# Optimization experiments

Measured on AMD Instinct MI355X. Metric: run time of the kernel, lower is better.

Reference implementation:

```python
import jax, jax.numpy as jnp
import numpy as np

HALF = 24576          # per-side HalfKP features (64 king sq * 6 piece * 64 sq)
NUMEL = 2 * HALF      # util.half_kp_numel()
BASE = 128
B = 8192


def _linear(x, W, b):
    return x @ W.T + b


def setup_inputs() -> dict:
    key = jax.random.key(0)
    ks = jax.random.split(key, 16)
    s = 0.01
    return {
        "pov": jax.random.uniform(ks[0], (B, 1), dtype=jnp.float32),
        "white": jax.random.uniform(ks[1], (B, HALF), dtype=jnp.float32),
        "black": jax.random.uniform(ks[2], (B, HALF), dtype=jnp.float32),
        "w_aff_W": jax.random.normal(ks[3], (BASE, NUMEL), dtype=jnp.float32) * s,
        "w_aff_b": jax.random.normal(ks[4], (BASE,), dtype=jnp.float32) * s,
        "b_aff_W": jax.random.normal(ks[5], (BASE, NUMEL), dtype=jnp.float32) * s,
        "b_aff_b": jax.random.normal(ks[6], (BASE,), dtype=jnp.float32) * s,
        "fc0_W": jax.random.normal(ks[7], (32, 2 * BASE), dtype=jnp.float32) * s,
        "fc0_b": jax.random.normal(ks[8], (32,), dtype=jnp.float32) * s,
        "fc1_W": jax.random.normal(ks[9], (32, 32), dtype=jnp.float32) * s,
        "fc1_b": jax.random.normal(ks[10], (32,), dtype=jnp.float32) * s,
        "fc2_W": jax.random.normal(ks[11], (32, 64), dtype=jnp.float32) * s,
        "fc2_b": jax.random.normal(ks[12], (32,), dtype=jnp.float32) * s,
        "fc3_W": jax.random.normal(ks[13], (1, 96), dtype=jnp.float32) * s,
        "fc3_b": jax.random.normal(ks[14], (1,), dtype=jnp.float32) * s,
    }


def reference(pov, white, black, w_aff_W, w_aff_b, b_aff_W, b_aff_b,
              fc0_W, fc0_b, fc1_W, fc1_b, fc2_W, fc2_b, fc3_W, fc3_b):
    # util.half_kp(a, b) = cat([a, b], dim=1)
    w_feat = jnp.concatenate([white, black], axis=1)  # [B, NUMEL]
    b_feat = jnp.concatenate([black, white], axis=1)
    w_ = _linear(w_feat, w_aff_W, w_aff_b)            # [B, 128]
    b_ = _linear(b_feat, b_aff_W, b_aff_b)
    wb = jnp.concatenate([w_, b_], axis=1)            # [B, 256]
    bw = jnp.concatenate([b_, w_], axis=1)
    base = jax.nn.relu(pov * wb + (1.0 - pov) * bw)
    x = jax.nn.relu(_linear(base, fc0_W, fc0_b))      # [B, 32]
    x = jnp.concatenate([x, jax.nn.relu(_linear(x, fc1_W, fc1_b))], axis=1)  # [B, 64]
    x = jnp.concatenate([x, jax.nn.relu(_linear(x, fc2_W, fc2_b))], axis=1)  # [B, 96]
    return _linear(x, fc3_W, fc3_b)                   # [B, 1]
```

## Files before the change

kernel.cpp:

```cpp
#include <hip/hip_runtime.h>
#include <hip/hip_bf16.h>
#include <stdint.h>

typedef float f32x4 __attribute__((ext_vector_type(4)));
typedef float fvec4 __attribute__((ext_vector_type(4)));
typedef short bf16x8 __attribute__((ext_vector_type(8)));

#define HALF_K 24576
#define NUMELK 49152
#define BATCH  8192
#define BM 128
#define BN 256
#define BK 64

__device__ __forceinline__ short f2bf(float f) {
  __hip_bfloat16 h = __float2bfloat16(f);
  return __builtin_bit_cast(short, h);
}

__device__ __forceinline__ void gload_lds16(const short* g, short* l) {
  __builtin_amdgcn_global_load_lds(
      (const __attribute__((address_space(1))) unsigned*)g,
      (__attribute__((address_space(3))) unsigned*)l, 16, 0, 0);
}
__device__ __forceinline__ void gload_lds16f(const float* g, float* l) {
  __builtin_amdgcn_global_load_lds(
      (const __attribute__((address_space(1))) unsigned*)g,
      (__attribute__((address_space(3))) unsigned*)l, 16, 0, 0);
}

__global__ __launch_bounds__(256)
void nnue_prep(const float* __restrict__ wW, const float* __restrict__ bW,
               short* __restrict__ Bprep) {
  int gid = blockIdx.x * 256 + threadIdx.x;
  int KT  = gid >> 11;
  int rem = gid & 2047;
  int col = rem >> 3;
  int kc  = rem & 7;
  int kg  = KT * 64 + kc * 8;
  const float* src;
  if (col < 128) {
    src = wW + (size_t)col * NUMELK + kg;
  } else {
    int kk = (kg < HALF_K) ? (kg + HALF_K) : (kg - HALF_K);
    src = bW + (size_t)(col - 128) * NUMELK + kk;
  }
  fvec4 v0 = ((const fvec4*)src)[0];
  fvec4 v1 = ((const fvec4*)src)[1];
  bf16x8 o;
  o[0] = f2bf(v0[0]); o[1] = f2bf(v0[1]); o[2] = f2bf(v0[2]); o[3] = f2bf(v0[3]);
  o[4] = f2bf(v1[0]); o[5] = f2bf(v1[1]); o[6] = f2bf(v1[2]); o[7] = f2bf(v1[3]);
  *(bf16x8*)(Bprep + (size_t)KT * 16384 + col * 64 + ((kc ^ (col & 7)) << 3)) = o;
}

__global__ __launch_bounds__(512, 4)
void nnue_gemm(const float* __restrict__ white, const float* __restrict__ black,
               const short* __restrict__ Bprep, float* __restrict__ partial,
               int kchunk, int S) {
  __shared__ float Alds[BM * BK];
  __shared__ short Blds[BN * BK];

  const int t    = threadIdx.x;
  const int lane = t & 63;
  const int wid  = t >> 6;

  const int bid = blockIdx.x;
  const int xcd = bid & 7, bi = bid >> 3;
  const int xpk = 8 / S;
  const int ks  = xcd / xpk;
  const int mt  = (xcd % xpk) * (64 / xpk) + bi;
  const int m0  = mt * BM;
  const int k0  = ks * kchunk;

  f32x4 acc[4][4];
  const f32x4 zero = {0.f, 0.f, 0.f, 0.f};
#pragma unroll
  for (int a = 0; a < 4; ++a)
#pragma unroll
    for (int b = 0; b < 4; ++b) acc[a][b] = zero;

  const int wm = wid >> 2, wn = wid & 3;
  const int l15 = lane & 15, l4 = lane >> 4;
  const int achunk = lane & 15;
  const int arsub  = lane >> 4;

  auto issueDMA = [&](int kg) {
    const float* Af; int ka;
    if (kg < HALF_K) { Af = white; ka = kg; } else { Af = black; ka = kg - HALF_K; }
#pragma unroll
    for (int j = 0; j < 4; ++j) {
      int row = wid * 16 + j * 4 + arsub;
      int sc  = achunk ^ (row & 7);
      const float* src = Af + (size_t)(m0 + row) * HALF_K + ka + sc * 4;
      gload_lds16f(src, &Alds[(wid * 4 + j) * 256]);
    }
    const int KT = kg >> 6;
    const short* bsrc = Bprep + (size_t)KT * 16384 + wid * 2048 + lane * 8;
    short* bdst = &Blds[wid * 2048];
#pragma unroll
    for (int j = 0; j < 4; ++j)
      gload_lds16(bsrc + j * 512, bdst + j * 512);
  };

  auto compute = [&]() {
#pragma unroll
    for (int kstep = 0; kstep < 2; ++kstep) {
      const int kc = kstep * 4 + l4;
      bf16x8 bfr[4];
#pragma unroll
      for (int nf = 0; nf < 4; ++nf) {
        int col = wn * 64 + nf * 16 + l15;
        bfr[nf] = *(const bf16x8*)&Blds[col * 64 + ((kc ^ (col & 7)) << 3)];
      }
#pragma unroll
      for (int mf = 0; mf < 4; ++mf) {
        int r  = wm * 64 + mf * 16 + l15;
        int c1 = (2 * kc) ^ (r & 7);
        fvec4 lo = *(const fvec4*)&Alds[r * 64 + c1 * 4];
        fvec4 hi = *(const fvec4*)&Alds[r * 64 + (c1 ^ 1) * 4];
        bf16x8 af;
        af[0] = f2bf(lo[0]); af[1] = f2bf(lo[1]); af[2] = f2bf(lo[2]); af[3] = f2bf(lo[3]);
        af[4] = f2bf(hi[0]); af[5] = f2bf(hi[1]); af[6] = f2bf(hi[2]); af[7] = f2bf(hi[3]);
#pragma unroll
        for (int nf = 0; nf < 4; ++nf)
          acc[mf][nf] = __builtin_amdgcn_mfma_f32_16x16x32_bf16(af, bfr[nf], acc[mf][nf], 0, 0, 0);
      }
    }
  };

  const int niter = kchunk / BK;

  issueDMA(k0);
  __syncthreads();

  for (int kt = 0; kt < niter; ++kt) {
    compute();
    __syncthreads();
    if (kt + 1 < niter) issueDMA(k0 + (kt + 1) * BK);
    __syncthreads();
  }

  float* P = partial + ((size_t)ks * BATCH + m0) * 256;
#pragma unroll
  for (int mf = 0; mf < 4; ++mf) {
    int row = wm * 64 + mf * 16 + l4 * 4;
#pragma unroll
    for (int nf = 0; nf < 4; ++nf) {
      int col = wn * 64 + nf * 16 + l15;
#pragma unroll
      for (int rr = 0; rr < 4; ++rr)
        P[(size_t)(row + rr) * 256 + col] = acc[mf][nf][rr];
    }
  }
}

__global__ __launch_bounds__(256)
void nnue_tail(const float* __restrict__ partial, int S,
               const float* __restrict__ pov,
               const float* __restrict__ waffb, const float* __restrict__ baffb,
               const float* __restrict__ fc0W, const float* __restrict__ fc0b,
               const float* __restrict__ fc1W, const float* __restrict__ fc1b,
               const float* __restrict__ fc2W, const float* __restrict__ fc2b,
               const float* __restrict__ fc3W, const float* __restrict__ fc3b,
               float* __restrict__ out) {
  __shared__ float w0s[32 * 256];
  __shared__ float w1s[32 * 32];
  __shared__ float w2s[32 * 64];
  __shared__ float w3s[96];
  __shared__ float b0s[32], b1s[32], b2s[32];
  __shared__ float base_s[4][256];
  __shared__ float b3s;

  const int t = threadIdx.x;
  for (int i = t; i < 8192; i += 256) { int j = i >> 8, k = i & 255; w0s[(j << 8) | ((k + j) & 255)] = fc0W[i]; }
  for (int i = t; i < 1024; i += 256) { int j = i >> 5, k = i & 31;  w1s[(j << 5) | ((k + j) & 31)]  = fc1W[i]; }
  for (int i = t; i < 2048; i += 256) { int j = i >> 6, k = i & 63;  w2s[(j << 6) | ((k + j) & 63)]  = fc2W[i]; }
  if (t < 96) w3s[t] = fc3W[t];
  if (t < 32) { b0s[t] = fc0b[t]; b1s[t] = fc1b[t]; b2s[t] = fc2b[t]; }
  if (t == 0) b3s = fc3b[0];
  __syncthreads();

  const int wid = t >> 6, lane = t & 63;
  const int m = blockIdx.x * 4 + wid;
  const float pv = pov[m];

  float val[4];
  {
    const float* p = partial + (size_t)m * 256 + lane * 4;
    fvec4 a = *(const fvec4*)p;
    for (int s = 1; s < S; ++s) a += *(const fvec4*)(p + (size_t)s * BATCH * 256);
    const int c0 = lane * 4;
#pragma unroll
    for (int j = 0; j < 4; ++j) {
      int c = c0 + j;
      float bias = (c < 128) ? waffb[c] : baffb[c - 128];
      val[j] = a[j] + bias;
    }
  }
#pragma unroll
  for (int j = 0; j < 4; ++j) {
    float other = __shfl(val[j], lane ^ 32, 64);
    if (lane < 32) {
      int c = lane * 4 + j;
      float w = val[j], b = other;
      base_s[wid][c]       = fmaxf(pv * w + (1.f - pv) * b, 0.f);
      base_s[wid][c + 128] = fmaxf(pv * b + (1.f - pv) * w, 0.f);
    }
  }
  __syncthreads();

  const int j = lane & 31, half = lane >> 5;
  const float* bs = &base_s[wid][0];

  float s0 = 0.f;
  for (int k = 0; k < 128; ++k) {
    int kk = half * 128 + k;
    s0 += bs[kk] * w0s[(j << 8) | ((kk + j) & 255)];
  }
  s0 += __shfl(s0, lane ^ 32, 64);
  float x0 = fmaxf(s0 + b0s[j], 0.f);

  float s1 = 0.f;
  for (int k = 0; k < 32; ++k)
    s1 += __shfl(x0, k, 64) * w1s[(j << 5) | ((k + j) & 31)];
  float x1 = fmaxf(s1 + b1s[j], 0.f);

  float s2 = 0.f;
  for (int k = 0; k < 32; ++k) {
    s2 += __shfl(x0, k, 64) * w2s[(j << 6) | ((k + j) & 63)];
    s2 += __shfl(x1, k, 64) * w2s[(j << 6) | ((k + 32 + j) & 63)];
  }
  float x2 = fmaxf(s2 + b2s[j], 0.f);

  float s3 = 0.f;
  for (int k = 0; k < 32; ++k) {
    s3 += __shfl(x0, k, 64) * w3s[k];
    s3 += __shfl(x1, k, 64) * w3s[32 + k];
    s3 += __shfl(x2, k, 64) * w3s[64 + k];
  }
  if (lane == 0) out[m] = s3 + b3s;
}

extern "C" void kernel_launch(void* const* d_in, const int* in_sizes, int n_in,
                              void* d_out, int out_size, void* d_ws, size_t ws_size,
                              hipStream_t stream) {
  const float* pov   = (const float*)d_in[0];
  const float* white = (const float*)d_in[1];
  const float* black = (const float*)d_in[2];
  const float* wW    = (const float*)d_in[3];
  const float* wb    = (const float*)d_in[4];
  const float* bW    = (const float*)d_in[5];
  const float* bb    = (const float*)d_in[6];
  const float* fc0W  = (const float*)d_in[7];
  const float* fc0b  = (const float*)d_in[8];
  const float* fc1W  = (const float*)d_in[9];
  const float* fc1b  = (const float*)d_in[10];
  const float* fc2W  = (const float*)d_in[11];
  const float* fc2b  = (const float*)d_in[12];
  const float* fc3W  = (const float*)d_in[13];
  const float* fc3b  = (const float*)d_in[14];
  float* out = (float*)d_out;

  short* Bprep = (short*)d_ws;
  const size_t BWS_BYTES = (size_t)256 * NUMELK * 2;
  float* partial = (float*)((char*)d_ws + BWS_BYTES);
  const size_t PART1 = (size_t)BATCH * 256 * 4;

  int S = 8;
  if (ws_size < BWS_BYTES + 8 * PART1) S = 4;
  if (ws_size < BWS_BYTES + 4 * PART1) S = 2;
  if (ws_size < BWS_BYTES + 2 * PART1) S = 1;

  nnue_prep<<<dim3(6144), 256, 0, stream>>>(wW, bW, Bprep);
  nnue_gemm<<<dim3(64 * S), 512, 0, stream>>>(white, black, Bprep, partial, NUMELK / S, S);
  nnue_tail<<<dim3(BATCH / 4), 256, 0, stream>>>(partial, S, pov, wb, bb,
      fc0W, fc0b, fc1W, fc1b, fc2W, fc2b, fc3W, fc3b, out);
}
```

Baseline: 436.8 us.

## Load A tiles directly into registers and double-buffer B in LDS

The GEMM tile grows to 256 rows, and each wave now owns 32 full rows across all 256 columns. The fp32 activations are loaded straight from global memory into registers instead of staging through LDS. B is double-buffered in LDS, with explicit vmcnt waits and single barriers, so the next tile's loads overlap the current tile's MFMAs. This removes A's LDS traffic and one barrier per iteration. In exchange it raises register pressure (occupancy hint drops to 2) and halves the grid to 32*S blocks, which may leave CUs underused.

```diff
diff --git a/kernel.cpp b/kernel.cpp
--- a/kernel.cpp
+++ b/kernel.cpp
@@ -9,9 +9,14 @@
 #define HALF_K 24576
 #define NUMELK 49152
 #define BATCH  8192
-#define BM 128
+#define BM 256
 #define BN 256
 #define BK 64
+
+#define VMCNT_I(n) asm volatile("s_waitcnt vmcnt(" #n ")" ::: "memory")
+#define VMCNT(n) VMCNT_I(n)
+#define SCHEDB   __builtin_amdgcn_sched_barrier(0)
+#define SBAR     __builtin_amdgcn_s_barrier()
 
 __device__ __forceinline__ short f2bf(float f) {
   __hip_bfloat16 h = __float2bfloat16(f);
@@ -19,11 +24,6 @@
 }
 
 __device__ __forceinline__ void gload_lds16(const short* g, short* l) {
-  __builtin_amdgcn_global_load_lds(
-      (const __attribute__((address_space(1))) unsigned*)g,
-      (__attribute__((address_space(3))) unsigned*)l, 16, 0, 0);
-}
-__device__ __forceinline__ void gload_lds16f(const float* g, float* l) {
   __builtin_amdgcn_global_load_lds(
       (const __attribute__((address_space(1))) unsigned*)g,
       (__attribute__((address_space(3))) unsigned*)l, 16, 0, 0);
@@ -53,100 +53,121 @@
   *(bf16x8*)(Bprep + (size_t)KT * 16384 + col * 64 + ((kc ^ (col & 7)) << 3)) = o;
 }
 
-__global__ __launch_bounds__(512, 4)
+__global__ __launch_bounds__(512, 2)
 void nnue_gemm(const float* __restrict__ white, const float* __restrict__ black,
                const short* __restrict__ Bprep, float* __restrict__ partial,
                int kchunk, int S) {
-  __shared__ float Alds[BM * BK];
-  __shared__ short Blds[BN * BK];
+  __shared__ short B0s[BN * BK];
+  __shared__ short B1s[BN * BK];
 
   const int t    = threadIdx.x;
   const int lane = t & 63;
-  const int wid  = t >> 6;
+  const int w    = t >> 6;
 
   const int bid = blockIdx.x;
   const int xcd = bid & 7, bi = bid >> 3;
   const int xpk = 8 / S;
   const int ks  = xcd / xpk;
-  const int mt  = (xcd % xpk) * (64 / xpk) + bi;
+  const int mt  = (xcd % xpk) * (32 / xpk) + bi;
   const int m0  = mt * BM;
   const int k0  = ks * kchunk;
-
-  f32x4 acc[4][4];
+  const int KT0 = k0 / BK;
+
+  f32x4 acc[2][16];
   const f32x4 zero = {0.f, 0.f, 0.f, 0.f};
 #pragma unroll
-  for (int a = 0; a < 4; ++a)
-#pragma unroll
-    for (int b = 0; b < 4; ++b) acc[a][b] = zero;
-
-  const int wm = wid >> 2, wn = wid & 3;
+  for (int a = 0; a < 2; ++a)
+#pragma unroll
+    for (int b = 0; b < 16; ++b) acc[a][b] = zero;
+
   const int l15 = lane & 15, l4 = lane >> 4;
-  const int achunk = lane & 15;
-  const int arsub  = lane >> 4;
-
-  auto issueDMA = [&](int kg) {
+
+  const size_t arow_off = (size_t)(m0 + w * 32 + l15) * HALF_K + l4 * 8;
+
+  auto issueA = [&](fvec4* va, int kg) {
     const float* Af; int ka;
     if (kg < HALF_K) { Af = white; ka = kg; } else { Af = black; ka = kg - HALF_K; }
-#pragma unroll
-    for (int j = 0; j < 4; ++j) {
-      int row = wid * 16 + j * 4 + arsub;
-      int sc  = achunk ^ (row & 7);
-      const float* src = Af + (size_t)(m0 + row) * HALF_K + ka + sc * 4;
-      gload_lds16f(src, &Alds[(wid * 4 + j) * 256]);
-    }
-    const int KT = kg >> 6;
-    const short* bsrc = Bprep + (size_t)KT * 16384 + wid * 2048 + lane * 8;
-    short* bdst = &Blds[wid * 2048];
+    const float* base = Af + arow_off + ka;
+#pragma unroll
+    for (int mf = 0; mf < 2; ++mf)
+#pragma unroll
+      for (int s = 0; s < 2; ++s) {
+        const fvec4* p = (const fvec4*)(base + (size_t)mf * 16 * HALF_K + s * 32);
+        va[mf * 4 + s * 2]     = p[0];
+        va[mf * 4 + s * 2 + 1] = p[1];
+      }
+  };
+
+  auto issueB = [&](short* dst, int KT) {
+    const short* src = Bprep + (size_t)KT * 16384 + w * 2048 + lane * 8;
+    short* d = dst + w * 2048;
 #pragma unroll
     for (int j = 0; j < 4; ++j)
-      gload_lds16(bsrc + j * 512, bdst + j * 512);
+      gload_lds16(src + j * 512, d + j * 512);
   };
 
-  auto compute = [&]() {
-#pragma unroll
-    for (int kstep = 0; kstep < 2; ++kstep) {
-      const int kc = kstep * 4 + l4;
-      bf16x8 bfr[4];
-#pragma unroll
-      for (int nf = 0; nf < 4; ++nf) {
-        int col = wn * 64 + nf * 16 + l15;
-        bfr[nf] = *(const bf16x8*)&Blds[col * 64 + ((kc ^ (col & 7)) << 3)];
-      }
-#pragma unroll
-      for (int mf = 0; mf < 4; ++mf) {
-        int r  = wm * 64 + mf * 16 + l15;
-        int c1 = (2 * kc) ^ (r & 7);
-        fvec4 lo = *(const fvec4*)&Alds[r * 64 + c1 * 4];
-        fvec4 hi = *(const fvec4*)&Alds[r * 64 + (c1 ^ 1) * 4];
-        bf16x8 af;
-        af[0] = f2bf(lo[0]); af[1] = f2bf(lo[1]); af[2] = f2bf(lo[2]); af[3] = f2bf(lo[3]);
-        af[4] = f2bf(hi[0]); af[5] = f2bf(hi[1]); af[6] = f2bf(hi[2]); af[7] = f2bf(hi[3]);
-#pragma unroll
-        for (int nf = 0; nf < 4; ++nf)
-          acc[mf][nf] = __builtin_amdgcn_mfma_f32_16x16x32_bf16(af, bfr[nf], acc[mf][nf], 0, 0, 0);
+  auto compute = [&](const short* Bb, const fvec4* va) {
+#pragma unroll
+    for (int s = 0; s < 2; ++s) {
+      bf16x8 af[2];
+#pragma unroll
+      for (int mf = 0; mf < 2; ++mf) {
+        const fvec4 lo = va[mf * 4 + s * 2];
+        const fvec4 hi = va[mf * 4 + s * 2 + 1];
+        af[mf][0] = f2bf(lo[0]); af[mf][1] = f2bf(lo[1]);
+        af[mf][2] = f2bf(lo[2]); af[mf][3] = f2bf(lo[3]);
+        af[mf][4] = f2bf(hi[0]); af[mf][5] = f2bf(hi[1]);
+        af[mf][6] = f2bf(hi[2]); af[mf][7] = f2bf(hi[3]);
+      }
+      const int kc = s * 4 + l4;
+#pragma unroll
+      for (int nf = 0; nf < 16; ++nf) {
+        int col = nf * 16 + l15;
+        bf16x8 bf = *(const bf16x8*)&Bb[col * 64 + ((kc ^ (col & 7)) << 3)];
+        acc[0][nf] = __builtin_amdgcn_mfma_f32_16x16x32_bf16(af[0], bf, acc[0][nf], 0, 0, 0);
+        acc[1][nf] = __builtin_amdgcn_mfma_f32_16x16x32_bf16(af[1], bf, acc[1][nf], 0, 0, 0);
       }
     }
   };
 
   const int niter = kchunk / BK;
 
-  issueDMA(k0);
-  __syncthreads();
-
-  for (int kt = 0; kt < niter; ++kt) {
-    compute();
-    __syncthreads();
-    if (kt + 1 < niter) issueDMA(k0 + (kt + 1) * BK);
-    __syncthreads();
+  fvec4 vaA[8], vaB[8];
+
+  issueB(B0s, KT0);
+  issueA(vaA, k0);
+  VMCNT(8); SCHEDB;
+  SBAR; SCHEDB;
+
+  for (int i = 0; i < niter; i += 2) {
+    if (i + 1 < niter) {
+      issueB(B1s, KT0 + i + 1);
+      issueA(vaB, k0 + (i + 1) * BK);
+    }
+    SCHEDB;
+    compute(B0s, vaA);
+    VMCNT(8); SCHEDB;
+    SBAR; SCHEDB;
+
+    if (i + 1 < niter) {
+      if (i + 2 < niter) {
+        issueB(B0s, KT0 + i + 2);
+        issueA(vaA, k0 + (i + 2) * BK);
+      }
+      SCHEDB;
+      compute(B1s, vaB);
+      VMCNT(8); SCHEDB;
+      SBAR; SCHEDB;
+    }
   }
 
   float* P = partial + ((size_t)ks * BATCH + m0) * 256;
 #pragma unroll
-  for (int mf = 0; mf < 4; ++mf) {
-    int row = wm * 64 + mf * 16 + l4 * 4;
-#pragma unroll
-    for (int nf = 0; nf < 4; ++nf) {
-      int col = wn * 64 + nf * 16 + l15;
+  for (int mf = 0; mf < 2; ++mf) {
+    int row = w * 32 + mf * 16 + l4 * 4;
+#pragma unroll
+    for (int nf = 0; nf < 16; ++nf) {
+      int col = nf * 16 + l15;
 #pragma unroll
       for (int rr = 0; rr < 4; ++rr)
         P[(size_t)(row + rr) * 256 + col] = acc[mf][nf][rr];
@@ -272,7 +293,7 @@
   if (ws_size < BWS_BYTES + 2 * PART1) S = 1;
 
   nnue_prep<<<dim3(6144), 256, 0, stream>>>(wW, bW, Bprep);
-  nnue_gemm<<<dim3(64 * S), 512, 0, stream>>>(white, black, Bprep, partial, NUMELK / S, S);
+  nnue_gemm<<<dim3(32 * S), 512, 0, stream>>>(white, black, Bprep, partial, NUMELK / S, S);
   nnue_tail<<<dim3(BATCH / 4), 256, 0, stream>>>(partial, S, pov, wb, bb,
       fc0W, fc0b, fc1W, fc1b, fc2W, fc2b, fc3W, fc3b, out);
 }
```

Measured after the change: 442.7 us. Within noise of the previous version (+1.4%).

## Pipeline GEMM with register-staged bf16 A tiles and double-buffered B in LDS

Applied to the files above, without the earlier changes.

Restructures the main GEMM loop. A is loaded through registers in 256-wide K chunks and converted to bf16 once before being written to LDS with a new swizzle. B is double-buffered in LDS so that loads for the next 64-K step overlap with MFMA compute, using explicit vmcnt waits and sched barriers. This removes the per-fragment fp32 to bf16 conversion in the inner loop and the load-compute serialization of the old single-buffer scheme. The cost is more LDS and more registers, so occupancy drops to 2 blocks per CU, and it assumes kchunk is a multiple of 256.

```diff
diff --git a/kernel.cpp b/kernel.cpp
--- a/kernel.cpp
+++ b/kernel.cpp
@@ -5,13 +5,21 @@
 typedef float f32x4 __attribute__((ext_vector_type(4)));
 typedef float fvec4 __attribute__((ext_vector_type(4)));
 typedef short bf16x8 __attribute__((ext_vector_type(8)));
+typedef short bf16x4 __attribute__((ext_vector_type(4)));
 
 #define HALF_K 24576
 #define NUMELK 49152
 #define BATCH  8192
 #define BM 128
 #define BN 256
+#define KOUT 256
 #define BK 64
+
+#define VMCNT_I(n) asm volatile("s_waitcnt vmcnt(" #n ")" ::: "memory")
+#define VMCNT(n) VMCNT_I(n)
+#define LGKM0    asm volatile("s_waitcnt lgkmcnt(0)" ::: "memory")
+#define SCHEDB   __builtin_amdgcn_sched_barrier(0)
+#define SBAR     __builtin_amdgcn_s_barrier()
 
 __device__ __forceinline__ short f2bf(float f) {
   __hip_bfloat16 h = __float2bfloat16(f);
@@ -19,11 +27,6 @@
 }
 
 __device__ __forceinline__ void gload_lds16(const short* g, short* l) {
-  __builtin_amdgcn_global_load_lds(
-      (const __attribute__((address_space(1))) unsigned*)g,
-      (__attribute__((address_space(3))) unsigned*)l, 16, 0, 0);
-}
-__device__ __forceinline__ void gload_lds16f(const float* g, float* l) {
   __builtin_amdgcn_global_load_lds(
       (const __attribute__((address_space(1))) unsigned*)g,
       (__attribute__((address_space(3))) unsigned*)l, 16, 0, 0);
@@ -53,16 +56,17 @@
   *(bf16x8*)(Bprep + (size_t)KT * 16384 + col * 64 + ((kc ^ (col & 7)) << 3)) = o;
 }
 
-__global__ __launch_bounds__(512, 4)
+__global__ __launch_bounds__(512, 2)
 void nnue_gemm(const float* __restrict__ white, const float* __restrict__ black,
                const short* __restrict__ Bprep, float* __restrict__ partial,
                int kchunk, int S) {
-  __shared__ float Alds[BM * BK];
-  __shared__ short Blds[BN * BK];
+  __shared__ short Alds[BM * KOUT];
+  __shared__ short Bb0[BN * BK];
+  __shared__ short Bb1[BN * BK];
 
   const int t    = threadIdx.x;
   const int lane = t & 63;
-  const int wid  = t >> 6;
+  const int w    = t >> 6;
 
   const int bid = blockIdx.x;
   const int xcd = bid & 7, bi = bid >> 3;
@@ -71,6 +75,7 @@
   const int mt  = (xcd % xpk) * (64 / xpk) + bi;
   const int m0  = mt * BM;
   const int k0  = ks * kchunk;
+  const int KT0 = k0 / BK;
 
   f32x4 acc[4][4];
   const f32x4 zero = {0.f, 0.f, 0.f, 0.f};
@@ -79,48 +84,58 @@
 #pragma unroll
     for (int b = 0; b < 4; ++b) acc[a][b] = zero;
 
-  const int wm = wid >> 2, wn = wid & 3;
+  const int wm = w >> 2, wn = w & 3;
   const int l15 = lane & 15, l4 = lane >> 4;
-  const int achunk = lane & 15;
-  const int arsub  = lane >> 4;
-
-  auto issueDMA = [&](int kg) {
+
+  fvec4 va[4][4];
+
+  auto issueA4 = [&](int g, int kg) {
     const float* Af; int ka;
     if (kg < HALF_K) { Af = white; ka = kg; } else { Af = black; ka = kg - HALF_K; }
-#pragma unroll
-    for (int j = 0; j < 4; ++j) {
-      int row = wid * 16 + j * 4 + arsub;
-      int sc  = achunk ^ (row & 7);
-      const float* src = Af + (size_t)(m0 + row) * HALF_K + ka + sc * 4;
-      gload_lds16f(src, &Alds[(wid * 4 + j) * 256]);
-    }
-    const int KT = kg >> 6;
-    const short* bsrc = Bprep + (size_t)KT * 16384 + wid * 2048 + lane * 8;
-    short* bdst = &Blds[wid * 2048];
+    const float* base = Af + ka + lane * 4;
+#pragma unroll
+    for (int jj = 0; jj < 4; ++jj) {
+      int r = (g * 4 + jj) * 8 + w;
+      va[g][jj] = *(const fvec4*)(base + (size_t)(m0 + r) * HALF_K);
+    }
+  };
+
+  auto issueB = [&](short* dst, int KT) {
+    const short* src = Bprep + (size_t)KT * 16384 + w * 2048 + lane * 8;
+    short* d = dst + w * 2048;
 #pragma unroll
     for (int j = 0; j < 4; ++j)
-      gload_lds16(bsrc + j * 512, bdst + j * 512);
+      gload_lds16(src + j * 512, d + j * 512);
   };
 
-  auto compute = [&]() {
-#pragma unroll
-    for (int kstep = 0; kstep < 2; ++kstep) {
-      const int kc = kstep * 4 + l4;
+  auto writeA = [&]() {
+    const int c = lane >> 1, h4 = (lane & 1) * 4;
+#pragma unroll
+    for (int g = 0; g < 4; ++g)
+#pragma unroll
+      for (int jj = 0; jj < 4; ++jj) {
+        int r = (g * 4 + jj) * 8 + w;
+        bf16x4 o;
+        o[0] = f2bf(va[g][jj][0]); o[1] = f2bf(va[g][jj][1]);
+        o[2] = f2bf(va[g][jj][2]); o[3] = f2bf(va[g][jj][3]);
+        *(bf16x4*)&Alds[r * 256 + ((c ^ (r & 15)) << 3) + h4] = o;
+      }
+  };
+
+  auto computeInner = [&](const short* Bb, int ki) {
+#pragma unroll
+    for (int s = 0; s < 2; ++s) {
+      const int kc = s * 4 + l4;
       bf16x8 bfr[4];
 #pragma unroll
       for (int nf = 0; nf < 4; ++nf) {
         int col = wn * 64 + nf * 16 + l15;
-        bfr[nf] = *(const bf16x8*)&Blds[col * 64 + ((kc ^ (col & 7)) << 3)];
+        bfr[nf] = *(const bf16x8*)&Bb[col * 64 + ((kc ^ (col & 7)) << 3)];
       }
 #pragma unroll
       for (int mf = 0; mf < 4; ++mf) {
-        int r  = wm * 64 + mf * 16 + l15;
-        int c1 = (2 * kc) ^ (r & 7);
-        fvec4 lo = *(const fvec4*)&Alds[r * 64 + c1 * 4];
-        fvec4 hi = *(const fvec4*)&Alds[r * 64 + (c1 ^ 1) * 4];
-        bf16x8 af;
-        af[0] = f2bf(lo[0]); af[1] = f2bf(lo[1]); af[2] = f2bf(lo[2]); af[3] = f2bf(lo[3]);
-        af[4] = f2bf(hi[0]); af[5] = f2bf(hi[1]); af[6] = f2bf(hi[2]); af[7] = f2bf(hi[3]);
+        int row = wm * 64 + mf * 16 + l15;
+        bf16x8 af = *(const bf16x8*)&Alds[row * 256 + (((ki * 8 + kc) ^ l15) << 3)];
 #pragma unroll
         for (int nf = 0; nf < 4; ++nf)
           acc[mf][nf] = __builtin_amdgcn_mfma_f32_16x16x32_bf16(af, bfr[nf], acc[mf][nf], 0, 0, 0);
@@ -128,16 +143,54 @@
     }
   };
 
-  const int niter = kchunk / BK;
-
-  issueDMA(k0);
-  __syncthreads();
-
-  for (int kt = 0; kt < niter; ++kt) {
-    compute();
-    __syncthreads();
-    if (kt + 1 < niter) issueDMA(k0 + (kt + 1) * BK);
-    __syncthreads();
+  const int nOut = kchunk / KOUT;
+
+  issueB(Bb0, KT0);
+#pragma unroll
+  for (int g = 0; g < 4; ++g) issueA4(g, k0);
+  VMCNT(0); SCHEDB;
+  writeA();
+  LGKM0; SBAR; SCHEDB;
+
+  for (int n = 0; n < nOut; ++n) {
+    const bool hn = (n + 1 < nOut);
+    const int kgN = k0 + (n + 1) * KOUT;
+    const int KTn = KT0 + n * 4;
+
+    issueB(Bb1, KTn + 1);
+    if (hn) issueA4(0, kgN);
+    SCHEDB;
+    computeInner(Bb0, 0);
+    if (hn) { VMCNT(4); } else { VMCNT(0); }
+    SCHEDB; SBAR; SCHEDB;
+
+    issueB(Bb0, KTn + 2);
+    if (hn) issueA4(1, kgN);
+    SCHEDB;
+    computeInner(Bb1, 1);
+    if (hn) { VMCNT(4); } else { VMCNT(0); }
+    SCHEDB; SBAR; SCHEDB;
+
+    issueB(Bb1, KTn + 3);
+    if (hn) issueA4(2, kgN);
+    SCHEDB;
+    computeInner(Bb0, 2);
+    if (hn) { VMCNT(4); } else { VMCNT(0); }
+    SCHEDB; SBAR; SCHEDB;
+
+    if (hn) {
+      issueB(Bb0, KTn + 4);
+      issueA4(3, kgN);
+    }
+    SCHEDB;
+    computeInner(Bb1, 3);
+    VMCNT(0);
+    SCHEDB; SBAR; SCHEDB;
+    if (hn) {
+      writeA();
+      LGKM0;
+    }
+    SBAR; SCHEDB;
   }
 
   float* P = partial + ((size_t)ks * BATCH + m0) * 256;
```

After: 478.9 us. 9.6% more time.
